# Performance work log

Measured on AMD Instinct MI355X. Metric: run time of the kernel, lower is better.

## Reference

```python
import jax, jax.numpy as jnp
import numpy as np

B, C_IN, C_MID, C_OUT, H, W = 256, 2, 128, 64, 15, 15
N_RES = 4  # line_length//2 - 1 with line_length=11

# per-direction input offsets for kernel taps w0 and w2 (w1 is always center),
# matching fix_direction_order=True sparse 3x3 kernel construction:
# dir0 horizontal, dir1 vertical, dir2 anti-diagonal, dir3 main diagonal.
OFFSETS = (((0, -1), (0, 1)),
           ((-1, 0), (1, 0)),
           ((1, -1), (-1, 1)),
           ((-1, -1), (1, 1)))


def shift2d(x, di, dj):
    # out[..., i, j] = x[..., i+di, j+dj] with zero padding (di,dj in {-1,0,1})
    nd = x.ndim
    xp = jnp.pad(x, [(0, 0)] * (nd - 2) + [(1, 1), (1, 1)])
    h, w = x.shape[-2], x.shape[-1]
    return xp[..., 1 + di:1 + di + h, 1 + dj:1 + dj + w]


def dir_conv(x, w, b):
    # x: [4,B,Cin,H,W]; w: [Cout,Cin,3]; b: [Cout]
    x0 = jnp.stack([shift2d(x[d], *OFFSETS[d][0]) for d in range(4)])
    x2 = jnp.stack([shift2d(x[d], *OFFSETS[d][1]) for d in range(4)])
    y = (jnp.einsum('oc,dbchw->dbohw', w[..., 0], x0)
         + jnp.einsum('oc,dbchw->dbohw', w[..., 1], x)
         + jnp.einsum('oc,dbchw->dbohw', w[..., 2], x2))
    return y + b[None, None, :, None, None]


def conv1x1(x, w, b):
    # x: [4,B,Cin,H,W]; w: [Cout,Cin]; b: [Cout]
    return jnp.einsum('oc,dbchw->dbohw', w, x) + b[None, None, :, None, None]


def setup_inputs() -> dict:
    key = jax.random.key(0)
    ks = jax.random.split(key, 16)
    s_in = 1.0 / np.sqrt(3 * C_IN)
    s_mid = 1.0 / np.sqrt(3 * C_MID)
    s_pw = 1.0 / np.sqrt(C_MID)
    return {
        'x': jax.random.normal(ks[0], (B, C_IN, H, W), jnp.float32),
        'dconv0_w': jax.random.normal(ks[1], (C_MID, C_IN, 3), jnp.float32) * s_in,
        'dconv0_b': jnp.zeros((C_MID,), jnp.float32),
        'res_dconv_w': jax.random.normal(ks[2], (N_RES, C_MID, C_MID, 3), jnp.float32) * s_mid,
        'res_dconv_b': jnp.zeros((N_RES, C_MID), jnp.float32),
        'res_pw_w': jax.random.normal(ks[3], (N_RES, C_MID, C_MID), jnp.float32) * s_pw,
        'res_pw_b': jnp.zeros((N_RES, C_MID), jnp.float32),
        'c0_w1': jax.random.normal(ks[4], (C_MID, C_MID), jnp.float32) * s_pw,
        'c0_b1': jnp.zeros((C_MID,), jnp.float32),
        'c0_w2': jax.random.normal(ks[5], (C_MID, C_MID), jnp.float32) * s_pw,
        'c0_b2': jnp.zeros((C_MID,), jnp.float32),
        'final_w': jax.random.normal(ks[6], (C_OUT, C_MID), jnp.float32) * s_pw,
        'final_b': jnp.zeros((C_OUT,), jnp.float32),
    }


def reference(x, dconv0_w, dconv0_b, res_dconv_w, res_dconv_b,
              res_pw_w, res_pw_b, c0_w1, c0_b1, c0_w2, c0_b2,
              final_w, final_b):
    act = jax.nn.silu
    # all 4 direction streams start from the same input plane
    h = jnp.broadcast_to(x[None], (4,) + x.shape)  # [4,B,Cin,H,W]
    h = act(dir_conv(h, dconv0_w, dconv0_b))
    # DirectionalConvResBlocks (norm='none')
    for i in range(N_RES):
        r = h
        h = act(dir_conv(h, res_dconv_w[i], res_dconv_b[i]))
        h = act(conv1x1(h, res_pw_w[i], res_pw_b[i]))
        h = h + r
    # Conv0dResBlock (two 1x1 convs, middle_dim_multipler=1)
    r = h
    h = act(conv1x1(h, c0_w1, c0_b1))
    h = act(conv1x1(h, c0_w2, c0_b2))
    h = h + r
    # final 1x1 conv, then stack directions at dim=1 -> [B,4,Cout,H,W]
    h = conv1x1(h, final_w, final_b)
    return jnp.transpose(h, (1, 0, 2, 3, 4))
```

## Files before the change

### kernel.cpp

```cpp
#include <hip/hip_runtime.h>

using u16 = unsigned short;
using u32 = unsigned int;

typedef __bf16 bf16x8 __attribute__((ext_vector_type(8)));
typedef float  f32x4  __attribute__((ext_vector_type(4)));

#define NPOS   225
#define NTIL   15
#define ROWP   136
#define A_ROWS 289
#define B_ROWS 241
#define A_ELEMS (A_ROWS*ROWP)
#define B_ELEMS (B_ROWS*ROWP)
#define LDS_BYTES ((A_ELEMS + B_ELEMS)*2)

#define WA_PER_L 49152
#define WP_OFF   (4*WA_PER_L)
#define WP_PER   16384
#define WF_OFF   (WP_OFF + 6*WP_PER)
#define W_U16_TOTAL (WF_OFF + 8192)

__device__ __forceinline__ float bflo(u32 q){ return __uint_as_float(q << 16); }
__device__ __forceinline__ float bfhi(u32 q){ return __uint_as_float(q & 0xffff0000u); }
__device__ __forceinline__ u16 f2bf(float f){
  u32 u = __float_as_uint(f);
  return (u16)((u + 0x7fffu + ((u >> 16) & 1u)) >> 16);
}
__device__ __forceinline__ u32 packbf(float a, float b){
  return (u32)f2bf(a) | ((u32)f2bf(b) << 16);
}
__device__ __forceinline__ float silu_f(float x){
  return x * __builtin_amdgcn_rcpf(1.f + __expf(-x));
}
__device__ __forceinline__ f32x4 mfma16(bf16x8 a, bf16x8 b, f32x4 c){
  return __builtin_amdgcn_mfma_f32_16x16x32_bf16(a, b, c, 0, 0, 0);
}

__global__ void prep_w(const float* __restrict__ d0w, const float* __restrict__ rdw,
                       const float* __restrict__ rpw, const float* __restrict__ c1w,
                       const float* __restrict__ c2w, const float* __restrict__ fw,
                       float* __restrict__ ws)
{
  u16* wsb = (u16*)(ws + 768);
  const int total = 768 + W_U16_TOTAL;
  for (int idx = blockIdx.x*blockDim.x + threadIdx.x; idx < total; idx += gridDim.x*blockDim.x){
    if (idx < 768){
      int k = idx >> 7, o = idx & 127;
      ws[idx] = d0w[o*6 + k];
      continue;
    }
    int e = idx - 768;
    float v;
    if (e < WP_OFF){
      int L = e / WA_PER_L, r = e % WA_PER_L;
      int w = r / 6144, r2 = r % 6144;
      int t = r2 >> 11, r3 = r2 & 2047;
      int kb = r3 >> 9, r4 = r3 & 511;
      int l = r4 >> 3, j = r4 & 7;
      int o = w*16 + (l & 15);
      int c = kb*32 + ((l >> 4) << 3) + j;
      v = rdw[((L*128 + o)*128 + c)*3 + t];
    } else if (e < WF_OFF){
      int t2 = e - WP_OFF;
      int i = t2 / WP_PER, r = t2 % WP_PER;
      int w = r >> 11, r2 = r & 2047;
      int kb = r2 >> 9, r3 = r2 & 511;
      int l = r3 >> 3, j = r3 & 7;
      int o = w*16 + (l & 15);
      int c = kb*32 + ((l >> 4) << 3) + j;
      v = (i < 4) ? rpw[(i*128 + o)*128 + c]
        : (i == 4) ? c1w[o*128 + c] : c2w[o*128 + c];
    } else {
      int e2 = e - WF_OFF;
      int ot = e2 >> 11, r = e2 & 2047;
      int kb = r >> 9, r2 = r & 511;
      int l = r2 >> 3, j = r2 & 7;
      int o = ot*16 + (l & 15);
      int c = kb*32 + ((l >> 4) << 3) + j;
      v = fw[o*128 + c];
    }
    wsb[e] = f2bf(v);
  }
}

__device__ __forceinline__ void dconv_mfma(const u16* __restrict__ As, u16* __restrict__ Bs,
    const u16* __restrict__ wloc, const float* __restrict__ bias,
    int lane, int ob, int off0, int off2)
{
  const int col = lane & 15, kg = lane >> 4, koff = kg*8;
  bf16x8 wa[3][4];
  #pragma unroll
  for (int t=0;t<3;++t)
    #pragma unroll
    for (int kb=0;kb<4;++kb)
      wa[t][kb] = *(const bf16x8*)(wloc + ((t*4+kb)*64 + lane)*8);
  f32x4 bias4 = *(const f32x4*)(bias + ob + kg*4);
  const int offr[3] = {off0, 0, off2};
  #pragma unroll 1
  for (int tile=0; tile<NTIL; ++tile){
    int p = tile*16 + col;
    int i = p/15, j = p - i*15;
    int rb = ((i+1)*17 + (j+1))*ROWP;
    f32x4 acc = bias4;
    #pragma unroll
    for (int t=0;t<3;++t){
      const u16* s = As + rb + offr[t] + koff;
      #pragma unroll
      for (int kb=0;kb<4;++kb)
        acc = mfma16(wa[t][kb], *(const bf16x8*)(s + kb*32), acc);
    }
    u16* dp = Bs + p*ROWP + ob + kg*4;
    uint2 v; v.x = packbf(silu_f(acc[0]), silu_f(acc[1]));
    v.y = packbf(silu_f(acc[2]), silu_f(acc[3]));
    *(uint2*)dp = v;
  }
}

template<bool SRC_HALO, bool DST_HALO, bool RESID>
__device__ __forceinline__ void pw_mfma(const u16* __restrict__ src, u16* __restrict__ dst,
    const u16* __restrict__ wloc, const float* __restrict__ bias, int lane, int ob)
{
  const int col = lane & 15, kg = lane >> 4, koff = kg*8;
  bf16x8 wp[4];
  #pragma unroll
  for (int kb=0;kb<4;++kb) wp[kb] = *(const bf16x8*)(wloc + (kb*64 + lane)*8);
  f32x4 bias4 = *(const f32x4*)(bias + ob + kg*4);
  #pragma unroll 1
  for (int tile=0; tile<NTIL; ++tile){
    int p = tile*16 + col;
    int i = p/15, j = p - i*15;
    int rsrc = SRC_HALO ? ((i+1)*17 + (j+1))*ROWP : p*ROWP;
    int rdst = DST_HALO ? ((i+1)*17 + (j+1))*ROWP : p*ROWP;
    f32x4 acc = bias4;
    #pragma unroll
    for (int kb=0;kb<4;++kb)
      acc = mfma16(wp[kb], *(const bf16x8*)(src + rsrc + kb*32 + koff), acc);
    u16* dp = dst + rdst + ob + kg*4;
    float s0 = silu_f(acc[0]), s1 = silu_f(acc[1]);
    float s2 = silu_f(acc[2]), s3 = silu_f(acc[3]);
    if (RESID){
      uint2 r = *(const uint2*)dp;
      s0 += bflo(r.x); s1 += bfhi(r.x); s2 += bflo(r.y); s3 += bfhi(r.y);
    }
    if (!DST_HALO || p < NPOS){
      uint2 v; v.x = packbf(s0, s1); v.y = packbf(s2, s3);
      *(uint2*)dp = v;
    }
  }
}

__global__ void __launch_bounds__(512)
mix9_main(const float* __restrict__ x,
          const float* __restrict__ b_d0,
          const float* __restrict__ b_rd,
          const float* __restrict__ b_rp,
          const float* __restrict__ b_c1,
          const float* __restrict__ b_c2,
          const float* __restrict__ b_fin,
          const float* __restrict__ wt,
          float* __restrict__ out)
{
  extern __shared__ u16 sm[];
  u16* As = sm;
  u16* Bs = sm + A_ELEMS;

  const int blk  = blockIdx.x;
  const int b    = blk >> 2, d = blk & 3;
  const int tid  = threadIdx.x;
  const int wave = __builtin_amdgcn_readfirstlane(tid >> 6);
  const int lane = tid & 63;
  const int ob   = wave * 16;
  const int col  = lane & 15, kg = lane >> 4;

  const int DI0[4] = {0,-1, 1,-1}, DJ0[4] = {-1, 0,-1,-1};
  const int DI2[4] = {0, 1,-1, 1}, DJ2[4] = { 1, 0, 1, 1};
  const int di0 = DI0[d], dj0 = DJ0[d], di2 = DI2[d], dj2 = DJ2[d];
  const int off0 = (di0*17 + dj0)*ROWP;
  const int off2 = (di2*17 + dj2)*ROWP;

  for (int k2 = tid; k2 < A_ELEMS; k2 += 512) As[k2] = 0;
  float* xs = (float*)Bs;
  for (int k2 = tid; k2 < 2*NPOS; k2 += 512) xs[k2] = x[b*(2*NPOS) + k2];
  __syncthreads();

  #pragma unroll 1
  for (int pb = 0; pb < 4; ++pb){
    int p = pb*64 + lane;
    if (p >= NPOS) continue;
    int i = p/15, j = p - i*15;
    float acc[16];
    #pragma unroll
    for (int oo=0;oo<16;++oo) acc[oo] = b_d0[ob+oo];
    #pragma unroll
    for (int c=0;c<2;++c){
      int i0=i+di0, j0=j+dj0, i2=i+di2, j2=j+dj2;
      float x0 = ((unsigned)i0<15u && (unsigned)j0<15u) ? xs[c*NPOS + i0*15 + j0] : 0.f;
      float x1 = xs[c*NPOS + p];
      float x2 = ((unsigned)i2<15u && (unsigned)j2<15u) ? xs[c*NPOS + i2*15 + j2] : 0.f;
      const float* w0r = wt + (c*3+0)*128 + ob;
      const float* w1r = wt + (c*3+1)*128 + ob;
      const float* w2r = wt + (c*3+2)*128 + ob;
      #pragma unroll
      for (int oo=0;oo<16;++oo)
        acc[oo] = fmaf(w0r[oo],x0, fmaf(w1r[oo],x1, fmaf(w2r[oo],x2, acc[oo])));
    }
    u16* dp = As + ((i+1)*17 + (j+1))*ROWP + ob;
    #pragma unroll
    for (int oo=0;oo<16;oo+=2)
      *(u32*)(dp+oo) = packbf(silu_f(acc[oo]), silu_f(acc[oo+1]));
  }
  __syncthreads();

  const u16* wsb = (const u16*)(wt + 768);

  #pragma unroll 1
  for (int L = 0; L < 4; ++L){
    dconv_mfma(As, Bs, wsb + L*WA_PER_L + wave*6144, b_rd + L*128, lane, ob, off0, off2);
    __syncthreads();
    pw_mfma<false,true,true>(Bs, As, wsb + WP_OFF + L*WP_PER + wave*2048, b_rp + L*128, lane, ob);
    __syncthreads();
  }

  pw_mfma<true,false,false>(As, Bs, wsb + WP_OFF + 4*WP_PER + wave*2048, b_c1, lane, ob);
  __syncthreads();
  pw_mfma<false,true,true>(Bs, As, wsb + WP_OFF + 5*WP_PER + wave*2048, b_c2, lane, ob);
  __syncthreads();

  {
    const int ot = wave & 3;
    const u16* wl = wsb + WF_OFF + ot*2048;
    bf16x8 wf[4];
    #pragma unroll
    for (int kb=0;kb<4;++kb) wf[kb] = *(const bf16x8*)(wl + (kb*64 + lane)*8);
    f32x4 bias4 = *(const f32x4*)(b_fin + ot*16 + kg*4);
    const int t0 = (wave < 4) ? 0 : 8;
    const int t1 = (wave < 4) ? 8 : NTIL;
    const int koff = kg*8;
    #pragma unroll 1
    for (int tile = t0; tile < t1; ++tile){
      int p = tile*16 + col;
      int i = p/15, j = p - i*15;
      int rb = ((i+1)*17 + (j+1))*ROWP;
      f32x4 acc = bias4;
      #pragma unroll
      for (int kb=0;kb<4;++kb)
        acc = mfma16(wf[kb], *(const bf16x8*)(As + rb + kb*32 + koff), acc);
      if (p < NPOS){
        float* op = out + ((size_t)((b*4 + d)*64 + ot*16 + kg*4))*NPOS + p;
        op[0]      = acc[0];
        op[NPOS]   = acc[1];
        op[2*NPOS] = acc[2];
        op[3*NPOS] = acc[3];
      }
    }
  }
}

extern "C" void kernel_launch(void* const* d_in, const int* in_sizes, int n_in,
                              void* d_out, int out_size, void* d_ws, size_t ws_size,
                              hipStream_t stream)
{
  const float* x     = (const float*)d_in[0];
  const float* w_d0  = (const float*)d_in[1];
  const float* b_d0  = (const float*)d_in[2];
  const float* w_rd  = (const float*)d_in[3];
  const float* b_rd  = (const float*)d_in[4];
  const float* w_rp  = (const float*)d_in[5];
  const float* b_rp  = (const float*)d_in[6];
  const float* w_c1  = (const float*)d_in[7];
  const float* b_c1  = (const float*)d_in[8];
  const float* w_c2  = (const float*)d_in[9];
  const float* b_c2  = (const float*)d_in[10];
  const float* w_fin = (const float*)d_in[11];
  const float* b_fin = (const float*)d_in[12];
  float* wt  = (float*)d_ws;
  float* out = (float*)d_out;

  prep_w<<<128, 512, 0, stream>>>(w_d0, w_rd, w_rp, w_c1, w_c2, w_fin, wt);

  (void)hipFuncSetAttribute((const void*)mix9_main,
                            hipFuncAttributeMaxDynamicSharedMemorySize, LDS_BYTES);
  mix9_main<<<1024, 512, LDS_BYTES, stream>>>(x, b_d0, b_rd, b_rp, b_c1, b_c2, b_fin, wt, out);
}
```

Baseline: 268.2 us.

## Remap MFMA tiles to image rows and split output groups across wave pairs

Each wave now computes two 16-channel output tiles over half of the spatial tiles, so every B-operand LDS load feeds two MFMAs. Spatial tiles are aligned to image rows (16 columns, one padded), which removes the divide-by-15 index math and simplifies halo addressing. bf16 packing now uses native conversion, and launch bounds request two blocks per CU. Register pressure rises with 24 weight fragments per wave in the dconv stage, and padding each row to 16 columns wastes one of every 16 MFMA columns.

```diff
diff --git a/kernel.cpp b/kernel.cpp
--- a/kernel.cpp
+++ b/kernel.cpp
@@ -7,13 +7,14 @@
 typedef float  f32x4  __attribute__((ext_vector_type(4)));
 
 #define NPOS   225
-#define NTIL   15
+#define NT     15
 #define ROWP   136
 #define A_ROWS 289
 #define B_ROWS 241
 #define A_ELEMS (A_ROWS*ROWP)
 #define B_ELEMS (B_ROWS*ROWP)
 #define LDS_BYTES ((A_ELEMS + B_ELEMS)*2)
+#define RSTRIDE17 (17*ROWP)
 
 #define WA_PER_L 49152
 #define WP_OFF   (4*WA_PER_L)
@@ -28,7 +29,9 @@
   return (u16)((u + 0x7fffu + ((u >> 16) & 1u)) >> 16);
 }
 __device__ __forceinline__ u32 packbf(float a, float b){
-  return (u32)f2bf(a) | ((u32)f2bf(b) << 16);
+  union { __bf16 h[2]; u32 u; } r;
+  r.h[0] = (__bf16)a; r.h[1] = (__bf16)b;
+  return r.u;
 }
 __device__ __forceinline__ float silu_f(float x){
   return x * __builtin_amdgcn_rcpf(1.f + __expf(-x));
@@ -86,71 +89,92 @@
 
 __device__ __forceinline__ void dconv_mfma(const u16* __restrict__ As, u16* __restrict__ Bs,
     const u16* __restrict__ wloc, const float* __restrict__ bias,
-    int lane, int ob, int off0, int off2)
+    int lane, int og, int T0, int T1, int off0, int off2)
 {
   const int col = lane & 15, kg = lane >> 4, koff = kg*8;
-  bf16x8 wa[3][4];
+  bf16x8 wa[2][12];
   #pragma unroll
-  for (int t=0;t<3;++t)
-    #pragma unroll
-    for (int kb=0;kb<4;++kb)
-      wa[t][kb] = *(const bf16x8*)(wloc + ((t*4+kb)*64 + lane)*8);
-  f32x4 bias4 = *(const f32x4*)(bias + ob + kg*4);
-  const int offr[3] = {off0, 0, off2};
+  for (int ot=0; ot<2; ++ot)
+    #pragma unroll
+    for (int f=0; f<12; ++f)
+      wa[ot][f] = *(const bf16x8*)(wloc + (2*og+ot)*6144 + f*512 + lane*8);
+  f32x4 bz0 = *(const f32x4*)(bias + (2*og)*16 + kg*4);
+  f32x4 bz1 = *(const f32x4*)(bias + (2*og+1)*16 + kg*4);
+  const int c1 = (col+1)*ROWP;
   #pragma unroll 1
-  for (int tile=0; tile<NTIL; ++tile){
-    int p = tile*16 + col;
-    int i = p/15, j = p - i*15;
-    int rb = ((i+1)*17 + (j+1))*ROWP;
-    f32x4 acc = bias4;
-    #pragma unroll
-    for (int t=0;t<3;++t){
-      const u16* s = As + rb + offr[t] + koff;
-      #pragma unroll
-      for (int kb=0;kb<4;++kb)
-        acc = mfma16(wa[t][kb], *(const bf16x8*)(s + kb*32), acc);
-    }
-    u16* dp = Bs + p*ROWP + ob + kg*4;
-    uint2 v; v.x = packbf(silu_f(acc[0]), silu_f(acc[1]));
-    v.y = packbf(silu_f(acc[2]), silu_f(acc[3]));
-    *(uint2*)dp = v;
+  for (int tile=T0; tile<T1; ++tile){
+    int rb = (tile+1)*RSTRIDE17 + c1;
+    const u16* s0 = As + rb + off0 + koff;
+    const u16* s1 = As + rb + koff;
+    const u16* s2 = As + rb + off2 + koff;
+    f32x4 a0 = bz0, a1 = bz1;
+    #pragma unroll
+    for (int kb=0; kb<4; ++kb){
+      bf16x8 v0 = *(const bf16x8*)(s0 + kb*32);
+      bf16x8 v1 = *(const bf16x8*)(s1 + kb*32);
+      bf16x8 v2 = *(const bf16x8*)(s2 + kb*32);
+      a0 = mfma16(wa[0][kb],   v0, a0); a1 = mfma16(wa[1][kb],   v0, a1);
+      a0 = mfma16(wa[0][4+kb], v1, a0); a1 = mfma16(wa[1][4+kb], v1, a1);
+      a0 = mfma16(wa[0][8+kb], v2, a0); a1 = mfma16(wa[1][8+kb], v2, a1);
+    }
+    if (col < 15){
+      u16* dp = Bs + (tile*16+col)*ROWP + og*32 + kg*4;
+      uint2 w0; w0.x = packbf(silu_f(a0[0]), silu_f(a0[1]));
+      w0.y = packbf(silu_f(a0[2]), silu_f(a0[3]));
+      *(uint2*)dp = w0;
+      uint2 w1; w1.x = packbf(silu_f(a1[0]), silu_f(a1[1]));
+      w1.y = packbf(silu_f(a1[2]), silu_f(a1[3]));
+      *(uint2*)(dp+16) = w1;
+    }
   }
 }
 
 template<bool SRC_HALO, bool DST_HALO, bool RESID>
 __device__ __forceinline__ void pw_mfma(const u16* __restrict__ src, u16* __restrict__ dst,
-    const u16* __restrict__ wloc, const float* __restrict__ bias, int lane, int ob)
+    const u16* __restrict__ wloc, const float* __restrict__ bias,
+    int lane, int og, int T0, int T1)
 {
   const int col = lane & 15, kg = lane >> 4, koff = kg*8;
-  bf16x8 wp[4];
+  bf16x8 wp[2][4];
   #pragma unroll
-  for (int kb=0;kb<4;++kb) wp[kb] = *(const bf16x8*)(wloc + (kb*64 + lane)*8);
-  f32x4 bias4 = *(const f32x4*)(bias + ob + kg*4);
+  for (int ot=0; ot<2; ++ot)
+    #pragma unroll
+    for (int kb=0; kb<4; ++kb)
+      wp[ot][kb] = *(const bf16x8*)(wloc + (2*og+ot)*2048 + kb*512 + lane*8);
+  f32x4 bz0 = *(const f32x4*)(bias + (2*og)*16 + kg*4);
+  f32x4 bz1 = *(const f32x4*)(bias + (2*og+1)*16 + kg*4);
+  const int c1 = (col+1)*ROWP;
   #pragma unroll 1
-  for (int tile=0; tile<NTIL; ++tile){
-    int p = tile*16 + col;
-    int i = p/15, j = p - i*15;
-    int rsrc = SRC_HALO ? ((i+1)*17 + (j+1))*ROWP : p*ROWP;
-    int rdst = DST_HALO ? ((i+1)*17 + (j+1))*ROWP : p*ROWP;
-    f32x4 acc = bias4;
-    #pragma unroll
-    for (int kb=0;kb<4;++kb)
-      acc = mfma16(wp[kb], *(const bf16x8*)(src + rsrc + kb*32 + koff), acc);
-    u16* dp = dst + rdst + ob + kg*4;
-    float s0 = silu_f(acc[0]), s1 = silu_f(acc[1]);
-    float s2 = silu_f(acc[2]), s3 = silu_f(acc[3]);
-    if (RESID){
-      uint2 r = *(const uint2*)dp;
-      s0 += bflo(r.x); s1 += bfhi(r.x); s2 += bflo(r.y); s3 += bfhi(r.y);
-    }
-    if (!DST_HALO || p < NPOS){
-      uint2 v; v.x = packbf(s0, s1); v.y = packbf(s2, s3);
-      *(uint2*)dp = v;
-    }
-  }
-}
-
-__global__ void __launch_bounds__(512)
+  for (int tile=T0; tile<T1; ++tile){
+    int rsrc = SRC_HALO ? (tile+1)*RSTRIDE17 + c1 : (tile*16+col)*ROWP;
+    int rdst = DST_HALO ? (tile+1)*RSTRIDE17 + c1 : (tile*16+col)*ROWP;
+    const u16* s = src + rsrc + koff;
+    f32x4 a0 = bz0, a1 = bz1;
+    #pragma unroll
+    for (int kb=0; kb<4; ++kb){
+      bf16x8 v = *(const bf16x8*)(s + kb*32);
+      a0 = mfma16(wp[0][kb], v, a0);
+      a1 = mfma16(wp[1][kb], v, a1);
+    }
+    if (col < 15){
+      u16* dp = dst + rdst + og*32 + kg*4;
+      float s0 = silu_f(a0[0]), s1 = silu_f(a0[1]), s2 = silu_f(a0[2]), s3 = silu_f(a0[3]);
+      float t0 = silu_f(a1[0]), t1 = silu_f(a1[1]), t2 = silu_f(a1[2]), t3 = silu_f(a1[3]);
+      if (RESID){
+        uint2 r0 = *(const uint2*)dp;
+        uint2 r1 = *(const uint2*)(dp+16);
+        s0 += bflo(r0.x); s1 += bfhi(r0.x); s2 += bflo(r0.y); s3 += bfhi(r0.y);
+        t0 += bflo(r1.x); t1 += bfhi(r1.x); t2 += bflo(r1.y); t3 += bfhi(r1.y);
+      }
+      uint2 w0; w0.x = packbf(s0, s1); w0.y = packbf(s2, s3);
+      *(uint2*)dp = w0;
+      uint2 w1; w1.x = packbf(t0, t1); w1.y = packbf(t2, t3);
+      *(uint2*)(dp+16) = w1;
+    }
+  }
+}
+
+__global__ void __launch_bounds__(512, 2)
 mix9_main(const float* __restrict__ x,
           const float* __restrict__ b_d0,
           const float* __restrict__ b_rd,
@@ -170,8 +194,11 @@
   const int tid  = threadIdx.x;
   const int wave = __builtin_amdgcn_readfirstlane(tid >> 6);
   const int lane = tid & 63;
+  const int og   = wave >> 1;
+  const int ph   = wave & 1;
+  const int T0   = ph * 8;
+  const int T1   = ph ? NT : 8;
   const int ob   = wave * 16;
-  const int col  = lane & 15, kg = lane >> 4;
 
   const int DI0[4] = {0,-1, 1,-1}, DJ0[4] = {-1, 0,-1,-1};
   const int DI2[4] = {0, 1,-1, 1}, DJ2[4] = { 1, 0, 1, 1};
@@ -186,9 +213,9 @@
 
   #pragma unroll 1
   for (int pb = 0; pb < 4; ++pb){
-    int p = pb*64 + lane;
-    if (p >= NPOS) continue;
-    int i = p/15, j = p - i*15;
+    int pp = pb*64 + lane;
+    int i = pp >> 4, j = pp & 15;
+    if (i >= 15 || j >= 15) continue;
     float acc[16];
     #pragma unroll
     for (int oo=0;oo<16;++oo) acc[oo] = b_d0[ob+oo];
@@ -196,7 +223,7 @@
     for (int c=0;c<2;++c){
       int i0=i+di0, j0=j+dj0, i2=i+di2, j2=j+dj2;
       float x0 = ((unsigned)i0<15u && (unsigned)j0<15u) ? xs[c*NPOS + i0*15 + j0] : 0.f;
-      float x1 = xs[c*NPOS + p];
+      float x1 = xs[c*NPOS + i*15 + j];
       float x2 = ((unsigned)i2<15u && (unsigned)j2<15u) ? xs[c*NPOS + i2*15 + j2] : 0.f;
       const float* w0r = wt + (c*3+0)*128 + ob;
       const float* w1r = wt + (c*3+1)*128 + ob;
@@ -216,38 +243,35 @@
 
   #pragma unroll 1
   for (int L = 0; L < 4; ++L){
-    dconv_mfma(As, Bs, wsb + L*WA_PER_L + wave*6144, b_rd + L*128, lane, ob, off0, off2);
+    dconv_mfma(As, Bs, wsb + L*WA_PER_L, b_rd + L*128, lane, og, T0, T1, off0, off2);
     __syncthreads();
-    pw_mfma<false,true,true>(Bs, As, wsb + WP_OFF + L*WP_PER + wave*2048, b_rp + L*128, lane, ob);
+    pw_mfma<false,true,true>(Bs, As, wsb + WP_OFF + L*WP_PER, b_rp + L*128, lane, og, T0, T1);
     __syncthreads();
   }
 
-  pw_mfma<true,false,false>(As, Bs, wsb + WP_OFF + 4*WP_PER + wave*2048, b_c1, lane, ob);
+  pw_mfma<true,false,false>(As, Bs, wsb + WP_OFF + 4*WP_PER, b_c1, lane, og, T0, T1);
   __syncthreads();
-  pw_mfma<false,true,true>(Bs, As, wsb + WP_OFF + 5*WP_PER + wave*2048, b_c2, lane, ob);
+  pw_mfma<false,true,true>(Bs, As, wsb + WP_OFF + 5*WP_PER, b_c2, lane, og, T0, T1);
   __syncthreads();
 
   {
-    const int ot = wave & 3;
-    const u16* wl = wsb + WF_OFF + ot*2048;
+    const int col = lane & 15, kg = lane >> 4, koff = kg*8;
+    const u16* wl = wsb + WF_OFF + og*2048;
     bf16x8 wf[4];
     #pragma unroll
     for (int kb=0;kb<4;++kb) wf[kb] = *(const bf16x8*)(wl + (kb*64 + lane)*8);
-    f32x4 bias4 = *(const f32x4*)(b_fin + ot*16 + kg*4);
-    const int t0 = (wave < 4) ? 0 : 8;
-    const int t1 = (wave < 4) ? 8 : NTIL;
-    const int koff = kg*8;
+    f32x4 bias4 = *(const f32x4*)(b_fin + og*16 + kg*4);
+    const int c1 = (col+1)*ROWP;
     #pragma unroll 1
-    for (int tile = t0; tile < t1; ++tile){
-      int p = tile*16 + col;
-      int i = p/15, j = p - i*15;
-      int rb = ((i+1)*17 + (j+1))*ROWP;
+    for (int tile = T0; tile < T1; ++tile){
+      int rb = (tile+1)*RSTRIDE17 + c1;
+      const u16* s = As + rb + koff;
       f32x4 acc = bias4;
       #pragma unroll
       for (int kb=0;kb<4;++kb)
-        acc = mfma16(wf[kb], *(const bf16x8*)(As + rb + kb*32 + koff), acc);
-      if (p < NPOS){
-        float* op = out + ((size_t)((b*4 + d)*64 + ot*16 + kg*4))*NPOS + p;
+        acc = mfma16(wf[kb], *(const bf16x8*)(s + kb*32), acc);
+      if (col < 15){
+        float* op = out + ((size_t)((b*4 + d)*64 + og*16 + kg*4))*NPOS + tile*15 + col;
         op[0]      = acc[0];
         op[NPOS]   = acc[1];
         op[2*NPOS] = acc[2];
```

Measured after the change: 239.8 us. 10.6% less time.
